# Kernel tuning notes

Hardware: AMD Instinct MI355X
Metric: run time of the kernel (lower is better)

The kernel has to match this reference:

```python
import jax, jax.numpy as jnp
import numpy as np

P_DIM, M_DIM = 512, 768
PROJ, HID, NCLS = 512, 256, 2
EPS = 1e-5


def _bn_eval(x, g, b):
    # BatchNorm1d in eval mode with fresh buffers: running_mean=0, running_var=1
    return x / jnp.sqrt(1.0 + EPS) * g + b


def setup_inputs() -> dict:
    key = jax.random.key(0)
    ks = jax.random.split(key, 8)
    x = jax.random.normal(ks[0], (256, P_DIM + M_DIM), dtype=jnp.float32)
    W1 = jax.random.normal(ks[1], (PROJ, P_DIM * M_DIM), dtype=jnp.float32) * 0.002
    b1 = jnp.zeros((PROJ,), jnp.float32)
    ln_g = jnp.ones((PROJ,), jnp.float32)
    ln_b = jnp.zeros((PROJ,), jnp.float32)
    W2 = jax.random.normal(ks[2], (HID, PROJ), dtype=jnp.float32) * 0.04
    b2 = jnp.zeros((HID,), jnp.float32)
    bn1_g = jnp.ones((HID,), jnp.float32)
    bn1_b = jnp.zeros((HID,), jnp.float32)
    W3 = jax.random.normal(ks[3], (HID // 2, HID), dtype=jnp.float32) * 0.06
    b3 = jnp.zeros((HID // 2,), jnp.float32)
    bn2_g = jnp.ones((HID // 2,), jnp.float32)
    bn2_b = jnp.zeros((HID // 2,), jnp.float32)
    W4 = jax.random.normal(ks[4], (NCLS, HID // 2), dtype=jnp.float32) * 0.09
    b4 = jnp.zeros((NCLS,), jnp.float32)
    return dict(x=x, W1=W1, b1=b1, ln_g=ln_g, ln_b=ln_b, W2=W2, b2=b2,
                bn1_g=bn1_g, bn1_b=bn1_b, W3=W3, b3=b3,
                bn2_g=bn2_g, bn2_b=bn2_b, W4=W4, b4=b4)


def reference(x, W1, b1, ln_g, ln_b, W2, b2, bn1_g, bn1_b, W3, b3, bn2_g, bn2_b, W4, b4):
    p = x[:, :P_DIM]                     # [B, P]
    m = x[:, P_DIM:P_DIM + M_DIM]        # [B, M]
    # kron[b, i*M + j] = p[b,i]*m[b,j]; Linear(kron_flat) fused into one contraction
    W1r = W1.reshape(PROJ, P_DIM, M_DIM)
    fused = jnp.einsum('bp,bm,kpm->bk', p, m, W1r) + b1   # [B, PROJ]
    # LayerNorm + ReLU (dropout is identity in eval)
    mu = jnp.mean(fused, axis=-1, keepdims=True)
    var = jnp.var(fused, axis=-1, keepdims=True)
    h = (fused - mu) / jnp.sqrt(var + EPS) * ln_g + ln_b
    h = jax.nn.relu(h)
    # classifier MLP with BatchNorm1d (eval-mode buffers)
    h = jax.nn.relu(_bn_eval(h @ W2.T + b2, bn1_g, bn1_b))
    h = jax.nn.relu(_bn_eval(h @ W3.T + b3, bn2_g, bn2_b))
    logits = h @ W4.T + b4               # [B, NCLS]
    return logits
```

## Files before the change

kernel.cpp:

```cpp
#include <hip/hip_runtime.h>
#include <hip/hip_bf16.h>

typedef __attribute__((ext_vector_type(4))) float f32x4;
typedef __attribute__((ext_vector_type(16))) float f32x16;
typedef __attribute__((ext_vector_type(8))) short short8;
typedef __attribute__((ext_vector_type(4))) short short4v;
typedef unsigned short ushort_t;

#define BATCH 256
#define PDIM 512
#define MDIM 768
#define XCOLS 1280
#define PROJ 512
#define HID 256
#define KTOT (PDIM * MDIM)

#define BN 32
#define NT 16
#define PSPLIT 64
#define PI_PER 8
#define NJW 12
#define NSTEPS 96

__device__ __forceinline__ ushort_t f2bf(float f) {
  __hip_bfloat16 h = __float2bfloat16(f);
  return __builtin_bit_cast(ushort_t, h);
}
__device__ __forceinline__ float bf2f(ushort_t u) {
  union { unsigned int i; float f; } c;
  c.i = ((unsigned int)u) << 16;
  return c.f;
}

__global__ void prep_kernel(const float* __restrict__ x, ushort_t* __restrict__ mF) {
  int tid = blockIdx.x * blockDim.x + threadIdx.x;
  int nth = gridDim.x * blockDim.x;
  for (int c = tid; c < NJW * 8 * 4 * 64; c += nth) {
    int lane = c & 63;
    int ks = (c >> 6) & 3;
    int mf = (c >> 8) & 7;
    int jw = c >> 11;
    int row = mf * 32 + (lane & 31);
    int k0 = jw * 64 + ks * 16 + ((lane >> 5) << 3);
    const float* src = x + row * XCOLS + PDIM + k0;
    f32x4 v0 = *(const f32x4*)src;
    f32x4 v1 = *(const f32x4*)(src + 4);
    short8 o;
#pragma unroll
    for (int i = 0; i < 4; ++i) {
      o[i] = (short)f2bf(v0[i]);
      o[i + 4] = (short)f2bf(v1[i]);
    }
    ((short8*)mF)[c] = o;
  }
}

__global__ __launch_bounds__(256, 4)
void einsum_kernel(const float* __restrict__ W1, const ushort_t* __restrict__ mF,
                   const float* __restrict__ x, float* __restrict__ outp,
                   int atomic_mode) {
  __shared__ ushort_t Bf[2][2048];
  __shared__ float pl[PI_PER * BATCH];

  const int ntile = blockIdx.x & 15;
  const int ps    = blockIdx.x >> 4;
  const int pi0   = ps * PI_PER;
  const int n0    = ntile * BN;
  const int t     = threadIdx.x;
  const int lane  = t & 63;
  const int w     = t >> 6;

  {
    const float* xr = x + (size_t)t * XCOLS + pi0;
    f32x4 v0 = *(const f32x4*)xr;
    f32x4 v1 = *(const f32x4*)(xr + 4);
    pl[t]             = v0[0];
    pl[256 + t]       = v0[1];
    pl[512 + t]       = v0[2];
    pl[768 + t]       = v0[3];
    pl[1024 + t]      = v1[0];
    pl[1280 + t]      = v1[1];
    pl[1536 + t]      = v1[2];
    pl[1792 + t]      = v1[3];
  }

  const int r = t >> 3, q = t & 7;
  const float* wrow = W1 + (size_t)(n0 + r) * KTOT + (size_t)pi0 * MDIM;
  const int wb0 = (r * 128 + q * 8) ^ ((r & 7) << 4);
  const int wb1 = (r * 128 + 64 + q * 8) ^ ((r & 7) << 4);

  const int bb0 = ((lane & 31) * 128 + ((lane >> 5) << 4)) ^ ((lane & 7) << 4);

  const short8* mv = (const short8*)mF;
  const int mbase = w * 512 + lane;
  short8 ac0 = mv[mbase];
  short8 ac1 = mv[mbase + 64];
  short8 ac2 = mv[mbase + 128];
  short8 ac3 = mv[mbase + 192];
  short8 ac4 = mv[mbase + 256];
  short8 ac5 = mv[mbase + 320];
  short8 ac6 = mv[mbase + 384];
  short8 ac7 = mv[mbase + 448];

  f32x4 wv0 = __builtin_nontemporal_load((const f32x4*)(wrow + q * 4));
  f32x4 wv1 = __builtin_nontemporal_load((const f32x4*)(wrow + 32 + q * 4));

  f32x16 fa0, fa1;
#pragma unroll
  for (int i = 0; i < 16; ++i) { fa0[i] = 0.f; fa1[i] = 0.f; }

  for (int s = 0; s < NSTEPS; ++s) {
    const int s1 = (s + 1 < NSTEPS) ? s + 1 : 0;
    const int kk1 = (s1 & 7) * MDIM + (s1 >> 3) * 64;
    f32x4 nv0 = __builtin_nontemporal_load((const f32x4*)(wrow + kk1 + q * 4));
    f32x4 nv1 = __builtin_nontemporal_load((const f32x4*)(wrow + kk1 + 32 + q * 4));

    {
      short4v lo, hi;
#pragma unroll
      for (int i = 0; i < 4; ++i) {
        lo[i] = (short)f2bf(wv0[i]);
        hi[i] = (short)f2bf(wv1[i]);
      }
      char* bbase = (char*)&Bf[s & 1][0];
      *(short4v*)(bbase + wb0) = lo;
      *(short4v*)(bbase + wb1) = hi;
    }
    asm volatile("s_waitcnt lgkmcnt(0)" ::: "memory");
    __builtin_amdgcn_s_barrier();
    asm volatile("" ::: "memory");

    const char* rb = (const char*)&Bf[s & 1][0];
    short8 bv0 = *(const short8*)(rb + (bb0 ^ 0));
    short8 bv1 = *(const short8*)(rb + (bb0 ^ 32));
    short8 bv2 = *(const short8*)(rb + (bb0 ^ 64));
    short8 bv3 = *(const short8*)(rb + (bb0 ^ 96));
    const int pilc = s & 7;
    const float pa = pl[pilc * BATCH + w * 64 + (lane & 31)];
    const float pb = pl[pilc * BATCH + w * 64 + 32 + (lane & 31)];

#define GENMM(acA, acB, bv)                                          \
    {                                                                \
      short8 aA, aB;                                                 \
      _Pragma("unroll")                                              \
      for (int e = 0; e < 8; ++e) {                                  \
        aA[e] = (short)f2bf(pa * bf2f((ushort_t)acA[e]));            \
        aB[e] = (short)f2bf(pb * bf2f((ushort_t)acB[e]));            \
      }                                                              \
      fa0 = __builtin_amdgcn_mfma_f32_32x32x16_bf16(aA, bv, fa0, 0, 0, 0); \
      fa1 = __builtin_amdgcn_mfma_f32_32x32x16_bf16(aB, bv, fa1, 0, 0, 0); \
    }
    GENMM(ac0, ac4, bv0)
    GENMM(ac1, ac5, bv1)
    GENMM(ac2, ac6, bv2)
    GENMM(ac3, ac7, bv3)
#undef GENMM

    if ((s & 7) == 7) {
      int jn = (s >> 3) + 1;
      if (jn >= NJW) jn = 0;
      const short8* srcn = mv + jn * 2048;
      ac0 = srcn[mbase];
      ac1 = srcn[mbase + 64];
      ac2 = srcn[mbase + 128];
      ac3 = srcn[mbase + 192];
      ac4 = srcn[mbase + 256];
      ac5 = srcn[mbase + 320];
      ac6 = srcn[mbase + 384];
      ac7 = srcn[mbase + 448];
    }

    wv0 = nv0; wv1 = nv1;
  }

  const int col   = n0 + (lane & 31);
  const int rbase = w * 64 + ((lane >> 5) << 2);
  if (atomic_mode) {
#pragma unroll
    for (int rr = 0; rr < 16; ++rr) {
      int row = rbase + (rr & 3) + ((rr >> 2) << 3);
      atomicAdd(&outp[(size_t)row * PROJ + col], fa0[rr]);
      atomicAdd(&outp[(size_t)(row + 32) * PROJ + col], fa1[rr]);
    }
  } else {
    float* dst = outp + (size_t)ps * BATCH * PROJ;
#pragma unroll
    for (int rr = 0; rr < 16; ++rr) {
      int row = rbase + (rr & 3) + ((rr >> 2) << 3);
      dst[(size_t)row * PROJ + col] = fa0[rr];
      dst[(size_t)(row + 32) * PROJ + col] = fa1[rr];
    }
  }
}

__global__ __launch_bounds__(256)
void mlp_kernel(const float* __restrict__ part, int nps,
                const float* __restrict__ b1, const float* __restrict__ lng,
                const float* __restrict__ lnb, const float* __restrict__ W2,
                const float* __restrict__ b2, const float* __restrict__ g1,
                const float* __restrict__ bb1, const float* __restrict__ W3,
                const float* __restrict__ b3, const float* __restrict__ g2,
                const float* __restrict__ bb2, const float* __restrict__ W4,
                const float* __restrict__ b4, float* __restrict__ out) {
  __shared__ float h1[PROJ];
  __shared__ float h2[HID];
  __shared__ float h3[HID / 2];
  __shared__ float red[16];
  const int b = blockIdx.x, t = threadIdx.x;

  float f0 = 0.f, f1 = 0.f;
  const float* p0 = part + (size_t)b * PROJ + t;
#pragma unroll 4
  for (int s = 0; s < nps; ++s) {
    f0 += p0[0];
    f1 += p0[256];
    p0 += (size_t)BATCH * PROJ;
  }
  f0 += b1[t];
  f1 += b1[t + 256];

  float sum = f0 + f1, ss = f0 * f0 + f1 * f1;
#pragma unroll
  for (int o = 32; o > 0; o >>= 1) {
    sum += __shfl_xor(sum, o);
    ss  += __shfl_xor(ss, o);
  }
  const int wv = t >> 6, ln = t & 63;
  if (ln == 0) { red[wv] = sum; red[8 + wv] = ss; }
  __syncthreads();
  sum = red[0] + red[1] + red[2] + red[3];
  ss  = red[8] + red[9] + red[10] + red[11];
  float mu   = sum * (1.f / 512.f);
  float var  = ss * (1.f / 512.f) - mu * mu;
  float rstd = rsqrtf(var + 1e-5f);
  h1[t]       = fmaxf(0.f, (f0 - mu) * rstd * lng[t] + lnb[t]);
  h1[t + 256] = fmaxf(0.f, (f1 - mu) * rstd * lng[t + 256] + lnb[t + 256]);
  __syncthreads();

  const float bninv = rsqrtf(1.f + 1e-5f);
  {
    const f32x4* wr = (const f32x4*)(W2 + (size_t)t * PROJ);
    const f32x4* hv = (const f32x4*)h1;
    float a = 0.f;
#pragma unroll 4
    for (int i = 0; i < PROJ / 4; ++i) {
      f32x4 wq = wr[i], h = hv[i];
      a += wq[0] * h[0] + wq[1] * h[1] + wq[2] * h[2] + wq[3] * h[3];
    }
    h2[t] = fmaxf(0.f, (a + b2[t]) * bninv * g1[t] + bb1[t]);
  }
  __syncthreads();
  if (t < 128) {
    const f32x4* wr = (const f32x4*)(W3 + (size_t)t * HID);
    const f32x4* hv = (const f32x4*)h2;
    float a = 0.f;
#pragma unroll 4
    for (int i = 0; i < HID / 4; ++i) {
      f32x4 wq = wr[i], h = hv[i];
      a += wq[0] * h[0] + wq[1] * h[1] + wq[2] * h[2] + wq[3] * h[3];
    }
    h3[t] = fmaxf(0.f, (a + b3[t]) * bninv * g2[t] + bb2[t]);
  }
  __syncthreads();
  if (t < 2) {
    const float* wr = W4 + t * 128;
    float a = 0.f;
#pragma unroll 4
    for (int i = 0; i < 128; ++i) a += wr[i] * h3[i];
    out[b * 2 + t] = a + b4[t];
  }
}

extern "C" void kernel_launch(void* const* d_in, const int* in_sizes, int n_in,
                              void* d_out, int out_size, void* d_ws, size_t ws_size,
                              hipStream_t stream) {
  const float* x   = (const float*)d_in[0];
  const float* W1  = (const float*)d_in[1];
  const float* b1  = (const float*)d_in[2];
  const float* lng = (const float*)d_in[3];
  const float* lnb = (const float*)d_in[4];
  const float* W2  = (const float*)d_in[5];
  const float* b2  = (const float*)d_in[6];
  const float* g1  = (const float*)d_in[7];
  const float* bb1 = (const float*)d_in[8];
  const float* W3  = (const float*)d_in[9];
  const float* b3  = (const float*)d_in[10];
  const float* g2  = (const float*)d_in[11];
  const float* bb2 = (const float*)d_in[12];
  const float* W4  = (const float*)d_in[13];
  const float* b4  = (const float*)d_in[14];
  float* out = (float*)d_out;

  char* ws = (char*)d_ws;
  ushort_t* mF = (ushort_t*)ws;
  float* big   = (float*)(ws + 524288);

  size_t need = 524288 + (size_t)PSPLIT * BATCH * PROJ * 4;
  bool partial = ws_size >= need;

  hipLaunchKernelGGL(prep_kernel, dim3(256), dim3(256), 0, stream, x, mF);
  if (partial) {
    hipLaunchKernelGGL(einsum_kernel, dim3(NT * PSPLIT), dim3(256), 0, stream,
                       W1, mF, x, big, 0);
    hipLaunchKernelGGL(mlp_kernel, dim3(BATCH), dim3(256), 0, stream, big, PSPLIT,
                       b1, lng, lnb, W2, b2, g1, bb1, W3, b3, g2, bb2, W4, b4, out);
  } else {
    hipMemsetAsync(big, 0, (size_t)BATCH * PROJ * 4, stream);
    hipLaunchKernelGGL(einsum_kernel, dim3(NT * PSPLIT), dim3(256), 0, stream,
                       W1, mF, x, big, 1);
    hipLaunchKernelGGL(mlp_kernel, dim3(BATCH), dim3(256), 0, stream, big, 1,
                       b1, lng, lnb, W2, b2, g1, bb1, W3, b3, g2, bb2, W4, b4, out);
  }
}
```

Baseline: 226.1 us.

## Use 512-thread blocks with halved p-split and deeper W1 prefetch

```diff
diff --git a/kernel.cpp b/kernel.cpp
--- a/kernel.cpp
+++ b/kernel.cpp
@@ -17,10 +17,10 @@
 
 #define BN 32
 #define NT 16
-#define PSPLIT 64
-#define PI_PER 8
+#define PSPLIT 32
+#define PI_PER 16
 #define NJW 12
-#define NSTEPS 96
+#define NSTEPS 192
 
 __device__ __forceinline__ ushort_t f2bf(float f) {
   __hip_bfloat16 h = __float2bfloat16(f);
@@ -55,7 +55,7 @@
   }
 }
 
-__global__ __launch_bounds__(256, 4)
+__global__ __launch_bounds__(512, 4)
 void einsum_kernel(const float* __restrict__ W1, const ushort_t* __restrict__ mF,
                    const float* __restrict__ x, float* __restrict__ outp,
                    int atomic_mode) {
@@ -71,124 +71,95 @@
   const int w     = t >> 6;
 
   {
-    const float* xr = x + (size_t)t * XCOLS + pi0;
+    const int b = t & 255, half = t >> 8;
+    const float* xr = x + (size_t)b * XCOLS + pi0 + half * 8;
     f32x4 v0 = *(const f32x4*)xr;
     f32x4 v1 = *(const f32x4*)(xr + 4);
-    pl[t]             = v0[0];
-    pl[256 + t]       = v0[1];
-    pl[512 + t]       = v0[2];
-    pl[768 + t]       = v0[3];
-    pl[1024 + t]      = v1[0];
-    pl[1280 + t]      = v1[1];
-    pl[1536 + t]      = v1[2];
-    pl[1792 + t]      = v1[3];
-  }
-
-  const int r = t >> 3, q = t & 7;
-  const float* wrow = W1 + (size_t)(n0 + r) * KTOT + (size_t)pi0 * MDIM;
-  const int wb0 = (r * 128 + q * 8) ^ ((r & 7) << 4);
-  const int wb1 = (r * 128 + 64 + q * 8) ^ ((r & 7) << 4);
-
-  const int bb0 = ((lane & 31) * 128 + ((lane >> 5) << 4)) ^ ((lane & 7) << 4);
+#pragma unroll
+    for (int i = 0; i < 4; ++i) {
+      pl[(half * 8 + i) * BATCH + b]     = v0[i];
+      pl[(half * 8 + 4 + i) * BATCH + b] = v1[i];
+    }
+  }
+
+  const int r = t >> 4, q2 = t & 15;
+  const float* wrow = W1 + (size_t)(n0 + r) * KTOT + (size_t)pi0 * MDIM + q2 * 4;
+  const int wb = (((q2 >> 2) * 64) + (((q2 >> 1) & 1) << 5) + r) * 16 + ((q2 & 1) << 3);
 
   const short8* mv = (const short8*)mF;
-  const int mbase = w * 512 + lane;
+  const int mbase = w * 256 + lane;
   short8 ac0 = mv[mbase];
   short8 ac1 = mv[mbase + 64];
   short8 ac2 = mv[mbase + 128];
   short8 ac3 = mv[mbase + 192];
-  short8 ac4 = mv[mbase + 256];
-  short8 ac5 = mv[mbase + 320];
-  short8 ac6 = mv[mbase + 384];
-  short8 ac7 = mv[mbase + 448];
-
-  f32x4 wv0 = __builtin_nontemporal_load((const f32x4*)(wrow + q * 4));
-  f32x4 wv1 = __builtin_nontemporal_load((const f32x4*)(wrow + 32 + q * 4));
-
-  f32x16 fa0, fa1;
-#pragma unroll
-  for (int i = 0; i < 16; ++i) { fa0[i] = 0.f; fa1[i] = 0.f; }
+
+  f32x4 wv = __builtin_nontemporal_load((const f32x4*)wrow);
+  f32x4 nv = __builtin_nontemporal_load((const f32x4*)(wrow + MDIM));
+
+  f32x16 fa;
+#pragma unroll
+  for (int i = 0; i < 16; ++i) fa[i] = 0.f;
+
+  __syncthreads();
 
   for (int s = 0; s < NSTEPS; ++s) {
-    const int s1 = (s + 1 < NSTEPS) ? s + 1 : 0;
-    const int kk1 = (s1 & 7) * MDIM + (s1 >> 3) * 64;
-    f32x4 nv0 = __builtin_nontemporal_load((const f32x4*)(wrow + kk1 + q * 4));
-    f32x4 nv1 = __builtin_nontemporal_load((const f32x4*)(wrow + kk1 + 32 + q * 4));
+    int s2 = s + 2; if (s2 >= NSTEPS) s2 -= NSTEPS;
+    const int kk2 = (s2 & 15) * MDIM + (s2 >> 4) * 64;
+    f32x4 xv = __builtin_nontemporal_load((const f32x4*)(wrow + kk2));
 
     {
-      short4v lo, hi;
-#pragma unroll
-      for (int i = 0; i < 4; ++i) {
-        lo[i] = (short)f2bf(wv0[i]);
-        hi[i] = (short)f2bf(wv1[i]);
-      }
-      char* bbase = (char*)&Bf[s & 1][0];
-      *(short4v*)(bbase + wb0) = lo;
-      *(short4v*)(bbase + wb1) = hi;
+      short4v o;
+#pragma unroll
+      for (int i = 0; i < 4; ++i) o[i] = (short)f2bf(wv[i]);
+      *(short4v*)((char*)&Bf[s & 1][0] + wb) = o;
     }
     asm volatile("s_waitcnt lgkmcnt(0)" ::: "memory");
     __builtin_amdgcn_s_barrier();
     asm volatile("" ::: "memory");
 
-    const char* rb = (const char*)&Bf[s & 1][0];
-    short8 bv0 = *(const short8*)(rb + (bb0 ^ 0));
-    short8 bv1 = *(const short8*)(rb + (bb0 ^ 32));
-    short8 bv2 = *(const short8*)(rb + (bb0 ^ 64));
-    short8 bv3 = *(const short8*)(rb + (bb0 ^ 96));
-    const int pilc = s & 7;
-    const float pa = pl[pilc * BATCH + w * 64 + (lane & 31)];
-    const float pb = pl[pilc * BATCH + w * 64 + 32 + (lane & 31)];
-
-#define GENMM(acA, acB, bv)                                          \
-    {                                                                \
-      short8 aA, aB;                                                 \
-      _Pragma("unroll")                                              \
-      for (int e = 0; e < 8; ++e) {                                  \
-        aA[e] = (short)f2bf(pa * bf2f((ushort_t)acA[e]));            \
-        aB[e] = (short)f2bf(pb * bf2f((ushort_t)acB[e]));            \
-      }                                                              \
-      fa0 = __builtin_amdgcn_mfma_f32_32x32x16_bf16(aA, bv, fa0, 0, 0, 0); \
-      fa1 = __builtin_amdgcn_mfma_f32_32x32x16_bf16(aB, bv, fa1, 0, 0, 0); \
-    }
-    GENMM(ac0, ac4, bv0)
-    GENMM(ac1, ac5, bv1)
-    GENMM(ac2, ac6, bv2)
-    GENMM(ac3, ac7, bv3)
+    const short8* rb = (const short8*)&Bf[s & 1][0];
+    const float pa = pl[(s & 15) * BATCH + w * 32 + (lane & 31)];
+
+#define GENMM(ac, ks)                                                  \
+    {                                                                  \
+      short8 bv = rb[(ks) * 64 + lane];                                \
+      short8 aA;                                                       \
+      _Pragma("unroll")                                                \
+      for (int e = 0; e < 8; ++e)                                      \
+        aA[e] = (short)f2bf(pa * bf2f((ushort_t)ac[e]));               \
+      fa = __builtin_amdgcn_mfma_f32_32x32x16_bf16(aA, bv, fa, 0, 0, 0); \
+    }
+    GENMM(ac0, 0)
+    GENMM(ac1, 1)
+    GENMM(ac2, 2)
+    GENMM(ac3, 3)
 #undef GENMM
 
-    if ((s & 7) == 7) {
-      int jn = (s >> 3) + 1;
-      if (jn >= NJW) jn = 0;
-      const short8* srcn = mv + jn * 2048;
-      ac0 = srcn[mbase];
-      ac1 = srcn[mbase + 64];
-      ac2 = srcn[mbase + 128];
-      ac3 = srcn[mbase + 192];
-      ac4 = srcn[mbase + 256];
-      ac5 = srcn[mbase + 320];
-      ac6 = srcn[mbase + 384];
-      ac7 = srcn[mbase + 448];
-    }
-
-    wv0 = nv0; wv1 = nv1;
-  }
-
-  const int col   = n0 + (lane & 31);
-  const int rbase = w * 64 + ((lane >> 5) << 2);
+    if ((s & 15) == 15) {
+      int jn = (s >> 4) + 1; if (jn >= NJW) jn = 0;
+      const short8* srcn = mv + jn * 2048 + mbase;
+      ac0 = srcn[0];
+      ac1 = srcn[64];
+      ac2 = srcn[128];
+      ac3 = srcn[192];
+    }
+    wv = nv; nv = xv;
+  }
+
+  const int col = n0 + (lane & 31);
+  const int rb2 = w * 32 + ((lane >> 5) << 2);
   if (atomic_mode) {
 #pragma unroll
     for (int rr = 0; rr < 16; ++rr) {
-      int row = rbase + (rr & 3) + ((rr >> 2) << 3);
-      atomicAdd(&outp[(size_t)row * PROJ + col], fa0[rr]);
-      atomicAdd(&outp[(size_t)(row + 32) * PROJ + col], fa1[rr]);
+      int row = rb2 + (rr & 3) + ((rr >> 2) << 3);
+      atomicAdd(&outp[(size_t)row * PROJ + col], fa[rr]);
     }
   } else {
     float* dst = outp + (size_t)ps * BATCH * PROJ;
 #pragma unroll
     for (int rr = 0; rr < 16; ++rr) {
-      int row = rbase + (rr & 3) + ((rr >> 2) << 3);
-      dst[(size_t)row * PROJ + col] = fa0[rr];
-      dst[(size_t)(row + 32) * PROJ + col] = fa1[rr];
+      int row = rb2 + (rr & 3) + ((rr >> 2) << 3);
+      dst[(size_t)row * PROJ + col] = fa[rr];
     }
   }
 }
@@ -300,13 +271,13 @@
 
   hipLaunchKernelGGL(prep_kernel, dim3(256), dim3(256), 0, stream, x, mF);
   if (partial) {
-    hipLaunchKernelGGL(einsum_kernel, dim3(NT * PSPLIT), dim3(256), 0, stream,
+    hipLaunchKernelGGL(einsum_kernel, dim3(NT * PSPLIT), dim3(512), 0, stream,
                        W1, mF, x, big, 0);
     hipLaunchKernelGGL(mlp_kernel, dim3(BATCH), dim3(256), 0, stream, big, PSPLIT,
                        b1, lng, lnb, W2, b2, g1, bb1, W3, b3, g2, bb2, W4, b4, out);
   } else {
     hipMemsetAsync(big, 0, (size_t)BATCH * PROJ * 4, stream);
-    hipLaunchKernelGGL(einsum_kernel, dim3(NT * PSPLIT), dim3(256), 0, stream,
+    hipLaunchKernelGGL(einsum_kernel, dim3(NT * PSPLIT), dim3(512), 0, stream,
                        W1, mF, x, big, 1);
     hipLaunchKernelGGL(mlp_kernel, dim3(BATCH), dim3(256), 0, stream, big, 1,
                        b1, lng, lnb, W2, b2, g1, bb1, W3, b3, g2, bb2, W4, b4, out);
```

Result: slower. 235.0 us (+3.9%).
